# Kernel tuning notes

Measured on AMD Instinct MI355X. Metric: run time of the kernel, lower is better.

The kernel has to match this reference:

```python
import jax, jax.numpy as jnp
import numpy as np

EPS = 1e-12  # F.normalize clamp_min


def setup_inputs() -> dict:
    key = jax.random.key(0)
    k1, k2, k3, k4 = jax.random.split(key, 4)
    emb_dim = 64
    user_feat = jax.random.normal(k1, (4096, emb_dim), dtype=jnp.float32)
    seq_feat = jax.random.normal(k2, (2048, 32, emb_dim), dtype=jnp.float32)
    # nn.Linear(emb_dim, emb_dim): weight [out, in], bias [out]
    bound = 1.0 / np.sqrt(emb_dim)
    W = jax.random.uniform(k3, (emb_dim, emb_dim), dtype=jnp.float32, minval=-bound, maxval=bound)
    b = jax.random.uniform(k4, (emb_dim,), dtype=jnp.float32, minval=-bound, maxval=bound)
    return {"user_feat": user_feat, "seq_feat": seq_feat, "W": W, "b": b}


def reference(user_feat, seq_feat, W, b):
    D = seq_feat.shape[-1]
    sf = seq_feat.reshape(-1, D)                       # [M, D]
    M = sf.shape[0]
    # attention scores + L1 row-normalization (F.normalize p=1, dim=1)
    att = jnp.einsum('nd,md->nm', user_feat, sf)       # [N, M]
    att = att / jnp.maximum(jnp.sum(jnp.abs(att), axis=1, keepdims=True), EPS)
    # mean_m Linear(att[n,m] * sf[m]) == (att @ sf)/M @ W^T + b  (affine distributivity)
    agg = jnp.einsum('nm,md->nd', att, sf) / M         # [N, D]
    message_mean = agg @ W.T + b                        # [N, D]
    return user_feat + message_mean
```

## Files before the change

### kernel.cpp

```cpp
#include <hip/hip_runtime.h>
#include <hip/hip_bf16.h>

typedef __attribute__((ext_vector_type(8))) short short8v;
typedef __attribute__((ext_vector_type(4))) float f32x4;

#define N_ROWS 4096
#define M_ROWS 65536
#define DIM 64

#define AS1C(p) ((const __attribute__((address_space(1))) void*)(p))
#define AS3(p)  ((__attribute__((address_space(3))) void*)(p))

__device__ inline unsigned short f2bf(float f) {
  unsigned u = __float_as_uint(f);
  unsigned r = (u + 0x7FFFu + ((u >> 16) & 1u)) >> 16;
  return (unsigned short)r;
}
__device__ inline float bf2f(unsigned short s) {
  return __uint_as_float(((unsigned)s) << 16);
}

__global__ __launch_bounds__(256) void cvt_g_kernel(const float* __restrict__ sf,
                                                    unsigned short* __restrict__ sf16,
                                                    float* __restrict__ Gp) {
  __shared__ unsigned short tile[128 * DIM];
  const int tid = threadIdx.x;
  const size_t base = (size_t)blockIdx.x * 128 * DIM;

#pragma unroll
  for (int j = 0; j < 8; ++j) {
    const int e = tid * 4 + j * 1024;
    float4 v = *reinterpret_cast<const float4*>(sf + base + e);
    ushort4 o;
    o.x = f2bf(v.x); o.y = f2bf(v.y); o.z = f2bf(v.z); o.w = f2bf(v.w);
    *reinterpret_cast<ushort4*>(sf16 + base + e) = o;
    *reinterpret_cast<ushort4*>(&tile[e]) = o;
  }
  __syncthreads();

  const int d1 = (tid & 15) * 4;
  const int d2 = (tid >> 4) * 4;
  float acc[4][4];
#pragma unroll
  for (int i = 0; i < 4; ++i)
#pragma unroll
    for (int j = 0; j < 4; ++j) acc[i][j] = 0.f;

#pragma unroll 8
  for (int m = 0; m < 128; ++m) {
    ushort4 a4 = *reinterpret_cast<const ushort4*>(&tile[m * DIM + d1]);
    ushort4 b4 = *reinterpret_cast<const ushort4*>(&tile[m * DIM + d2]);
    float a[4] = {bf2f(a4.x), bf2f(a4.y), bf2f(a4.z), bf2f(a4.w)};
    float b[4] = {bf2f(b4.x), bf2f(b4.y), bf2f(b4.z), bf2f(b4.w)};
#pragma unroll
    for (int i = 0; i < 4; ++i)
#pragma unroll
      for (int j = 0; j < 4; ++j) acc[i][j] += a[i] * b[j];
  }
#pragma unroll
  for (int i = 0; i < 4; ++i)
#pragma unroll
    for (int j = 0; j < 4; ++j)
      Gp[(size_t)blockIdx.x * 4096 + (d1 + i) * DIM + (d2 + j)] = acc[i][j];
}

__global__ __launch_bounds__(256) void s_kernel(const float* __restrict__ u,
                                                const unsigned short* __restrict__ sf16,
                                                float* __restrict__ Spart) {
  __shared__ unsigned short Bt[2][8192];
  const int bn = blockIdx.x;
  const int bm = blockIdx.y;
  const int tid = threadIdx.x;
  const int wid = tid >> 6;
  const int lane = tid & 63;
  const int l15 = lane & 15;
  const int lg  = lane >> 4;
  const int n0 = bn * 512 + wid * 128;
  const int mbase = bm * 1024;

  short8v au[8][2];
#pragma unroll
  for (int st = 0; st < 8; ++st) {
#pragma unroll
    for (int kf = 0; kf < 2; ++kf) {
      const float* ap = u + (size_t)(n0 + st * 16 + l15) * DIM + kf * 32 + lg * 8;
      float4 f0 = *reinterpret_cast<const float4*>(ap);
      float4 f1 = *reinterpret_cast<const float4*>(ap + 4);
      short8v v;
      v[0] = (short)f2bf(f0.x); v[1] = (short)f2bf(f0.y);
      v[2] = (short)f2bf(f0.z); v[3] = (short)f2bf(f0.w);
      v[4] = (short)f2bf(f1.x); v[5] = (short)f2bf(f1.y);
      v[6] = (short)f2bf(f1.z); v[7] = (short)f2bf(f1.w);
      au[st][kf] = v;
    }
  }

  f32x4 sacc[8];
#pragma unroll
  for (int st = 0; st < 8; ++st) sacc[st] = (f32x4){0.f, 0.f, 0.f, 0.f};

#define STAGE(buf, step)                                                       \
  {                                                                            \
    _Pragma("unroll") for (int j = 0; j < 4; ++j) {                            \
      const int idx = wid * 4 + j;                                             \
      const int kp = idx >> 1;                                                 \
      const int h = idx & 1;                                                   \
      const unsigned short* g =                                                \
          sf16 + (size_t)(mbase + (step) * 128 + h * 64 + lane) * DIM + kp * 8;\
      __builtin_amdgcn_global_load_lds(AS1C(g), AS3(&Bt[buf][kp * 1024 + h * 512]), 16, 0, 0); \
    }                                                                          \
  }

  STAGE(0, 0);
  for (int s = 0; s < 8; ++s) {
    __syncthreads();
    if (s < 7) STAGE((s + 1) & 1, s + 1);
    const unsigned short* B = &Bt[s & 1][0];
#pragma unroll
    for (int g = 0; g < 8; ++g) {
      short8v b0 = *reinterpret_cast<const short8v*>(
          &B[(size_t)lg * 1024 + (g * 16 + l15) * 8]);
      short8v b1 = *reinterpret_cast<const short8v*>(
          &B[(size_t)(4 + lg) * 1024 + (g * 16 + l15) * 8]);
#pragma unroll
      for (int st = 0; st < 8; ++st) {
        f32x4 acc = (f32x4){0.f, 0.f, 0.f, 0.f};
        acc = __builtin_amdgcn_mfma_f32_16x16x32_bf16(au[st][0], b0, acc, 0, 0, 0);
        acc = __builtin_amdgcn_mfma_f32_16x16x32_bf16(au[st][1], b1, acc, 0, 0, 0);
        sacc[st][0] += fabsf(acc[0]);
        sacc[st][1] += fabsf(acc[1]);
        sacc[st][2] += fabsf(acc[2]);
        sacc[st][3] += fabsf(acc[3]);
      }
    }
  }
#undef STAGE

#pragma unroll
  for (int off = 1; off < 16; off <<= 1) {
#pragma unroll
    for (int st = 0; st < 8; ++st) {
#pragma unroll
      for (int r = 0; r < 4; ++r)
        sacc[st][r] += __shfl_xor(sacc[st][r], off, 64);
    }
  }
  if (l15 == 0) {
#pragma unroll
    for (int st = 0; st < 8; ++st)
#pragma unroll
      for (int r = 0; r < 4; ++r)
        Spart[(size_t)(n0 + st * 16 + lg * 4 + r) * 64 + bm] = sacc[st][r];
  }
}

__global__ __launch_bounds__(256) void gp_reduce_p(const float* __restrict__ Gp,
                                                   const float* __restrict__ W,
                                                   float* __restrict__ P) {
  const int j = blockIdx.x;
  const int d = threadIdx.x & 63;
  const int q = threadIdx.x >> 6;
  float g = 0.f;
#pragma unroll 8
  for (int i = 0; i < 128; ++i)
    g += Gp[(size_t)(q + 4 * i) * 4096 + j * DIM + d];
  __shared__ float part[4][DIM];
  part[q][d] = g;
  __syncthreads();
  if (q == 0) {
    float row = part[0][d] + part[1][d] + part[2][d] + part[3][d];
    part[0][d] = row;
  }
  __syncthreads();
  if (q == 0) {
    float acc = 0.f;
#pragma unroll
    for (int k = 0; k < DIM; ++k) acc += part[0][k] * W[d * DIM + k];
    P[j * DIM + d] = acc;
  }
}

__global__ __launch_bounds__(256) void out_kernel(const float* __restrict__ u,
                                                  const float* __restrict__ P,
                                                  const float* __restrict__ Spart,
                                                  const float* __restrict__ bias,
                                                  float* __restrict__ out) {
  __shared__ float Ps[DIM][DIM];
  __shared__ float us[4][DIM];
  const int tid = threadIdx.x;
#pragma unroll
  for (int i = 0; i < 16; ++i)
    (&Ps[0][0])[tid + i * 256] = P[tid + i * 256];
  const int base = blockIdx.x * 256;
  us[tid >> 6][tid & 63] = u[base + tid];
  __syncthreads();

  const int nl = tid >> 6;
  const int d = tid & 63;
  const int n = blockIdx.x * 4 + nl;

  float sp = Spart[(size_t)n * 64 + d];
#pragma unroll
  for (int off = 1; off < 64; off <<= 1) sp += __shfl_xor(sp, off, 64);
  const float inv = 1.f / (fmaxf(sp, 1e-12f) * (float)M_ROWS);

  float acc = 0.f;
#pragma unroll
  for (int jj = 0; jj < DIM; ++jj) acc += us[nl][jj] * Ps[jj][d];
  out[base + tid] = us[nl][d] + acc * inv + bias[d];
}

extern "C" void kernel_launch(void* const* d_in, const int* in_sizes, int n_in,
                              void* d_out, int out_size, void* d_ws, size_t ws_size,
                              hipStream_t stream) {
  const float* u  = (const float*)d_in[0];
  const float* sf = (const float*)d_in[1];
  const float* W  = (const float*)d_in[2];
  const float* b  = (const float*)d_in[3];
  float* out = (float*)d_out;

  char* ws = (char*)d_ws;
  unsigned short* sf16 = (unsigned short*)ws;
  float* Spart = (float*)(ws + 8388608);
  float* Gp    = (float*)(ws + 9437184);
  float* P     = (float*)(ws + 17825792);

  cvt_g_kernel<<<dim3(512), 256, 0, stream>>>(sf, sf16, Gp);
  s_kernel<<<dim3(8, 64), 256, 0, stream>>>(u, sf16, Spart);
  gp_reduce_p<<<dim3(64), 256, 0, stream>>>(Gp, W, P);
  out_kernel<<<dim3(N_ROWS * 64 / 256), 256, 0, stream>>>(u, P, Spart, b, out);
}
```

Before: 148.4 us.

## Restructure score kernel into 4-deep LDS ring with finer waitcnt pipelining

The score kernel now handles 64 rows per wave instead of 128 and doubles the grid to 16x64 blocks. Launch bounds now request 4 blocks per CU. The shared B tile is split into four 64-row buffers used as a ring with two loads in flight. Explicit vmcnt waits and sched barriers replace the full __syncthreads. The aim is higher occupancy and better overlap of global-to-LDS loads with MFMA work, at the cost of reloading each user-row block twice as often across the grid.

```diff
diff --git a/kernel.cpp b/kernel.cpp
--- a/kernel.cpp
+++ b/kernel.cpp
@@ -10,6 +10,7 @@
 
 #define AS1C(p) ((const __attribute__((address_space(1))) void*)(p))
 #define AS3(p)  ((__attribute__((address_space(3))) void*)(p))
+#define SCHED0() __builtin_amdgcn_sched_barrier(0)
 
 __device__ inline unsigned short f2bf(float f) {
   unsigned u = __float_as_uint(f);
@@ -64,10 +65,10 @@
       Gp[(size_t)blockIdx.x * 4096 + (d1 + i) * DIM + (d2 + j)] = acc[i][j];
 }
 
-__global__ __launch_bounds__(256) void s_kernel(const float* __restrict__ u,
-                                                const unsigned short* __restrict__ sf16,
-                                                float* __restrict__ Spart) {
-  __shared__ unsigned short Bt[2][8192];
+__global__ __launch_bounds__(256, 4) void s_kernel(const float* __restrict__ u,
+                                                   const unsigned short* __restrict__ sf16,
+                                                   float* __restrict__ Spart) {
+  __shared__ unsigned short Bt[4][4096];
   const int bn = blockIdx.x;
   const int bm = blockIdx.y;
   const int tid = threadIdx.x;
@@ -75,12 +76,12 @@
   const int lane = tid & 63;
   const int l15 = lane & 15;
   const int lg  = lane >> 4;
-  const int n0 = bn * 512 + wid * 128;
+  const int n0 = bn * 256 + wid * 64;
   const int mbase = bm * 1024;
 
-  short8v au[8][2];
-#pragma unroll
-  for (int st = 0; st < 8; ++st) {
+  short8v au[4][2];
+#pragma unroll
+  for (int st = 0; st < 4; ++st) {
 #pragma unroll
     for (int kf = 0; kf < 2; ++kf) {
       const float* ap = u + (size_t)(n0 + st * 16 + l15) * DIM + kf * 32 + lg * 8;
@@ -95,37 +96,49 @@
     }
   }
 
-  f32x4 sacc[8];
-#pragma unroll
-  for (int st = 0; st < 8; ++st) sacc[st] = (f32x4){0.f, 0.f, 0.f, 0.f};
+  f32x4 sacc[4];
+#pragma unroll
+  for (int st = 0; st < 4; ++st) sacc[st] = (f32x4){0.f, 0.f, 0.f, 0.f};
+  const f32x4 ZERO = (f32x4){0.f, 0.f, 0.f, 0.f};
 
 #define STAGE(buf, step)                                                       \
   {                                                                            \
-    _Pragma("unroll") for (int j = 0; j < 4; ++j) {                            \
-      const int idx = wid * 4 + j;                                             \
-      const int kp = idx >> 1;                                                 \
-      const int h = idx & 1;                                                   \
+    _Pragma("unroll") for (int j = 0; j < 2; ++j) {                            \
+      const int kp = wid * 2 + j;                                              \
       const unsigned short* g =                                                \
-          sf16 + (size_t)(mbase + (step) * 128 + h * 64 + lane) * DIM + kp * 8;\
-      __builtin_amdgcn_global_load_lds(AS1C(g), AS3(&Bt[buf][kp * 1024 + h * 512]), 16, 0, 0); \
+          sf16 + (size_t)(mbase + (step) * 64 + lane) * DIM + kp * 8;          \
+      __builtin_amdgcn_global_load_lds(AS1C(g),                                \
+          AS3(&Bt[0][0] + (size_t)(buf) * 4096 + kp * 512), 16, 0, 0);         \
     }                                                                          \
   }
 
   STAGE(0, 0);
-  for (int s = 0; s < 8; ++s) {
-    __syncthreads();
-    if (s < 7) STAGE((s + 1) & 1, s + 1);
-    const unsigned short* B = &Bt[s & 1][0];
-#pragma unroll
-    for (int g = 0; g < 8; ++g) {
+  STAGE(1, 1);
+
+  const int boff = l15 * 8;
+
+#pragma unroll 1
+  for (int s = 0; s < 16; ++s) {
+    SCHED0();
+    if (s < 15) {
+      asm volatile("s_waitcnt vmcnt(2)" ::: "memory");
+    } else {
+      asm volatile("s_waitcnt vmcnt(0)" ::: "memory");
+    }
+    SCHED0();
+    __builtin_amdgcn_s_barrier();
+    SCHED0();
+    if (s < 14) STAGE((s + 2) & 3, s + 2);
+    const unsigned short* B = &Bt[0][0] + (size_t)(s & 3) * 4096;
+#pragma unroll
+    for (int g = 0; g < 4; ++g) {
       short8v b0 = *reinterpret_cast<const short8v*>(
-          &B[(size_t)lg * 1024 + (g * 16 + l15) * 8]);
+          &B[(size_t)lg * 512 + g * 128 + boff]);
       short8v b1 = *reinterpret_cast<const short8v*>(
-          &B[(size_t)(4 + lg) * 1024 + (g * 16 + l15) * 8]);
-#pragma unroll
-      for (int st = 0; st < 8; ++st) {
-        f32x4 acc = (f32x4){0.f, 0.f, 0.f, 0.f};
-        acc = __builtin_amdgcn_mfma_f32_16x16x32_bf16(au[st][0], b0, acc, 0, 0, 0);
+          &B[(size_t)(4 + lg) * 512 + g * 128 + boff]);
+#pragma unroll
+      for (int st = 0; st < 4; ++st) {
+        f32x4 acc = __builtin_amdgcn_mfma_f32_16x16x32_bf16(au[st][0], b0, ZERO, 0, 0, 0);
         acc = __builtin_amdgcn_mfma_f32_16x16x32_bf16(au[st][1], b1, acc, 0, 0, 0);
         sacc[st][0] += fabsf(acc[0]);
         sacc[st][1] += fabsf(acc[1]);
@@ -139,7 +152,7 @@
 #pragma unroll
   for (int off = 1; off < 16; off <<= 1) {
 #pragma unroll
-    for (int st = 0; st < 8; ++st) {
+    for (int st = 0; st < 4; ++st) {
 #pragma unroll
       for (int r = 0; r < 4; ++r)
         sacc[st][r] += __shfl_xor(sacc[st][r], off, 64);
@@ -147,7 +160,7 @@
   }
   if (l15 == 0) {
 #pragma unroll
-    for (int st = 0; st < 8; ++st)
+    for (int st = 0; st < 4; ++st)
 #pragma unroll
       for (int r = 0; r < 4; ++r)
         Spart[(size_t)(n0 + st * 16 + lg * 4 + r) * 64 + bm] = sacc[st][r];
@@ -226,7 +239,7 @@
   float* P     = (float*)(ws + 17825792);
 
   cvt_g_kernel<<<dim3(512), 256, 0, stream>>>(sf, sf16, Gp);
-  s_kernel<<<dim3(8, 64), 256, 0, stream>>>(u, sf16, Spart);
+  s_kernel<<<dim3(16, 64), 256, 0, stream>>>(u, sf16, Spart);
   gp_reduce_p<<<dim3(64), 256, 0, stream>>>(Gp, W, P);
   out_kernel<<<dim3(N_ROWS * 64 / 256), 256, 0, stream>>>(u, P, Spart, b, out);
 }
```

After: 132.5 us. 10.7% less time.
